# Optimization experiments

Measured on AMD Instinct MI355X. Metric: run time of the kernel, lower is better.

Reference implementation:

```python
import jax, jax.numpy as jnp
import numpy as np

N = 131072      # number of nodes / samples
IN_DIM = 128    # input_dim
H = 128         # hidden_dim
OUT_DIM = 10    # output_dim


def setup_inputs() -> dict:
    key = jax.random.key(0)
    ks = jax.random.split(key, 20)
    s = 0.05
    def rn(k, shape):
        return jax.random.normal(k, shape, jnp.float32) * s
    return {
        "x": jax.random.normal(ks[0], (N, IN_DIM), jnp.float32),
        # GRU layer 1 (seq_len=1, h0=0 => weight_hh contributes nothing; only b_hh matters)
        "w_ih_f1": rn(ks[1], (3 * H, IN_DIM)), "b_ih_f1": rn(ks[2], (3 * H,)), "b_hh_f1": rn(ks[3], (3 * H,)),
        "w_ih_b1": rn(ks[4], (3 * H, IN_DIM)), "b_ih_b1": rn(ks[5], (3 * H,)), "b_hh_b1": rn(ks[6], (3 * H,)),
        # GRU layer 2 (input 2H)
        "w_ih_f2": rn(ks[7], (3 * H, 2 * H)), "b_ih_f2": rn(ks[8], (3 * H,)), "b_hh_f2": rn(ks[9], (3 * H,)),
        "w_ih_b2": rn(ks[10], (3 * H, 2 * H)), "b_ih_b2": rn(ks[11], (3 * H,)), "b_hh_b2": rn(ks[12], (3 * H,)),
        # GCNConv layers
        "w_g1": rn(ks[13], (2 * H, 128)), "b_g1": rn(ks[14], (128,)),
        "w_g2": rn(ks[15], (128, 64)), "b_g2": rn(ks[16], (64,)),
        # final fc
        "w_fc": rn(ks[17], (64, OUT_DIM)), "b_fc": rn(ks[18], (OUT_DIM,)),
    }


def _gru_cell_zero(x, w_ih, b_ih, b_hh):
    # PyTorch GRU cell with h_prev = 0: h' = (1 - z) * n_gate
    gi = x @ w_ih.T + b_ih                    # [n, 3H]
    ir, iz, inn = jnp.split(gi, 3, axis=-1)
    hr, hz, hn = jnp.split(b_hh, 3)
    r = jax.nn.sigmoid(ir + hr)
    z = jax.nn.sigmoid(iz + hz)
    ng = jnp.tanh(inn + r * hn)
    return (1.0 - z) * ng


def _gcn(x, w, b, sources, targets, n):
    # PyG GCNConv: D^{-1/2}(A+I)D^{-1/2} X W + b, self-loops already in edge lists
    xw = x @ w                                 # [n, out]
    deg = jax.ops.segment_sum(jnp.ones(sources.shape[0], x.dtype), targets, num_segments=n)
    dinv = jax.lax.rsqrt(deg)
    norm = dinv[sources] * dinv[targets]       # [E]
    msg = norm[:, None] * xw[sources]          # gather
    return jax.ops.segment_sum(msg, targets, num_segments=n) + b  # scatter-add


def reference(x, w_ih_f1, b_ih_f1, b_hh_f1, w_ih_b1, b_ih_b1, b_hh_b1,
              w_ih_f2, b_ih_f2, b_hh_f2, w_ih_b2, b_ih_b2, b_hh_b2,
              w_g1, b_g1, w_g2, b_g2, w_fc, b_fc):
    n = x.shape[0]
    # seq_len = 1 => bidirectional GRU output is [fwd_cell(x); bwd_cell(x)]
    h1 = jnp.concatenate([_gru_cell_zero(x, w_ih_f1, b_ih_f1, b_hh_f1),
                          _gru_cell_zero(x, w_ih_b1, b_ih_b1, b_hh_b1)], axis=-1)
    h2 = jnp.concatenate([_gru_cell_zero(h1, w_ih_f2, b_ih_f2, b_hh_f2),
                          _gru_cell_zero(h1, w_ih_b2, b_ih_b2, b_hh_b2)], axis=-1)
    # chain graph, both directions, plus self loops (GCNConv adds them)
    src = jnp.arange(n - 1)
    dst = jnp.arange(1, n)
    ar = jnp.arange(n)
    sources = jnp.concatenate([src, dst, ar])
    targets = jnp.concatenate([dst, src, ar])
    g1 = _gcn(h2, w_g1, b_g1, sources, targets, n)   # dropout is identity in eval
    g2 = _gcn(g1, w_g2, b_g2, sources, targets, n)
    return g2 @ w_fc + b_fc
```

## Files before the change

kernel.cpp:

```cpp
#include <hip/hip_runtime.h>
#include <stdint.h>

#define N_NODES 131072
#define HDIM 128

typedef __bf16 bf16x8 __attribute__((ext_vector_type(8)));
typedef float f32x4 __attribute__((ext_vector_type(4)));
typedef unsigned short ushort_t;

__device__ __forceinline__ ushort_t f2bf(float f) {
    union { float f; uint32_t i; } v; v.f = f;
    uint32_t i = v.i;
    return (ushort_t)((i + 0x7FFFu + ((i >> 16) & 1u)) >> 16);
}

__device__ __forceinline__ void gll16(const ushort_t* g, ushort_t* l) {
    __builtin_amdgcn_global_load_lds(
        (const __attribute__((address_space(1))) uint32_t*)g,
        (__attribute__((address_space(3))) uint32_t*)l, 16, 0, 0);
}

__device__ __forceinline__ bf16x8 ldsw(const ushort_t* base, int R, int g) {
    return *(const bf16x8*)&base[R * 64 + (((g - R) & 7) << 3)];
}

__device__ __forceinline__ float fsig(float x) {
    return __builtin_amdgcn_rcpf(1.0f + __expf(-x));
}
__device__ __forceinline__ float ftanh(float y) {
    float yc = fminf(fmaxf(y, -15.0f), 15.0f);
    float e = __expf(2.0f * yc);
    return (e - 1.0f) * __builtin_amdgcn_rcpf(e + 1.0f);
}

template<int NC>
__device__ __forceinline__ void swz(int b, int& m, int& c) {
    int mhi = b / (8 * NC);
    int rem = b - mhi * (8 * NC);
    c = rem >> 3;
    m = mhi * 8 + (rem & 7);
}

__global__ __launch_bounds__(256) void prep_all(
    const float* __restrict__ w_f1, const float* __restrict__ w_b1,
    const float* __restrict__ w_f2, const float* __restrict__ w_b2,
    ushort_t* __restrict__ PWF1, ushort_t* __restrict__ PWB1,
    ushort_t* __restrict__ PWF2, ushort_t* __restrict__ PWB2,
    const float* __restrict__ w_g1, const float* __restrict__ b_g1,
    const float* __restrict__ w_g2, const float* __restrict__ b_g2,
    const float* __restrict__ w_fc, const float* __restrict__ b_fc,
    ushort_t* __restrict__ M16, float* __restrict__ cc)
{
    __shared__ float wfc_s[640];
    __shared__ float T1[128][10];
    const int t = threadIdx.x;

    if (blockIdx.x < 1152) {
        int idx = blockIdx.x * 256 + t;
        if (idx < 49152) {
            PWF1[idx] = f2bf(w_f1[idx]);
        } else if (idx < 98304) {
            int j = idx - 49152;  PWB1[j] = f2bf(w_b1[j]);
        } else if (idx < 196608) {
            int j = idx - 98304;  PWF2[j] = f2bf(w_f2[j]);
        } else if (idx < 294912) {
            int j = idx - 196608; PWB2[j] = f2bf(w_b2[j]);
        }
        return;
    }

    for (int i = t; i < 640; i += 256) wfc_s[i] = w_fc[i];
    __syncthreads();
    if (t < 128) {
        float s[10];
        #pragma unroll
        for (int j = 0; j < 10; ++j) s[j] = 0.0f;
        const float4* row = (const float4*)(w_g2 + t * 64);
        #pragma unroll
        for (int k4 = 0; k4 < 16; ++k4) {
            float4 v = row[k4];
            #pragma unroll
            for (int j = 0; j < 10; ++j)
                s[j] += v.x * wfc_s[(k4 * 4 + 0) * 10 + j] + v.y * wfc_s[(k4 * 4 + 1) * 10 + j]
                      + v.z * wfc_s[(k4 * 4 + 2) * 10 + j] + v.w * wfc_s[(k4 * 4 + 3) * 10 + j];
        }
        #pragma unroll
        for (int j = 0; j < 10; ++j) T1[t][j] = s[j];
    }
    __syncthreads();
    float m[10];
    #pragma unroll
    for (int j = 0; j < 10; ++j) m[j] = 0.0f;
    const float4* row1 = (const float4*)(w_g1 + t * 128);
    #pragma unroll 4
    for (int k4 = 0; k4 < 32; ++k4) {
        float4 v = row1[k4];
        #pragma unroll
        for (int j = 0; j < 10; ++j)
            m[j] += v.x * T1[k4 * 4 + 0][j] + v.y * T1[k4 * 4 + 1][j]
                  + v.z * T1[k4 * 4 + 2][j] + v.w * T1[k4 * 4 + 3][j];
    }
    #pragma unroll
    for (int j = 0; j < 16; ++j)
        M16[j * 256 + t] = (j < 10) ? f2bf(m[j]) : (ushort_t)0;
    if (t < 10) {
        float s1 = 0.0f;
        for (int k2 = 0; k2 < 128; ++k2) s1 += b_g1[k2] * T1[k2][t];
        cc[t] = s1;
        float s2 = 0.0f;
        for (int k3 = 0; k3 < 64; ++k3) s2 += b_g2[k3] * wfc_s[k3 * 10 + t];
        cc[16 + t] = s2 + b_fc[t];
    }
}

__global__ __launch_bounds__(256, 5) void gru_l1(
    const float* __restrict__ X,
    const ushort_t* __restrict__ Wf,
    const ushort_t* __restrict__ Wb,
    const float* __restrict__ bi_f, const float* __restrict__ bh_f,
    const float* __restrict__ bi_b, const float* __restrict__ bh_b,
    ushort_t* __restrict__ Hout)
{
    __shared__ ushort_t As[128 * 64];
    __shared__ ushort_t Bs[96 * 64];
    const int tid = threadIdx.x;
    int mt, comb;
    swz<8>(blockIdx.x, mt, comb);
    const int m0 = mt * 128;
    const int dir = comb >> 2;
    const int j0 = (comb & 3) * 32;
    const ushort_t* W = dir ? Wb : Wf;
    const float* b_ih = dir ? bi_b : bi_f;
    const float* b_hh = dir ? bh_b : bh_f;
    const int coloff = dir << 7;

    const int wv = tid >> 6, lane = tid & 63;
    const int lr = lane & 15, lq = lane >> 4;
    const int tr = tid >> 3, tc = tid & 7;
    const int sc = ((tr + tc) & 7) << 3;

    f32x4 acc[3][2][2];
    #pragma unroll
    for (int g = 0; g < 3; ++g)
        #pragma unroll
        for (int rt = 0; rt < 2; ++rt)
            #pragma unroll
            for (int ct = 0; ct < 2; ++ct)
                #pragma unroll
                for (int e = 0; e < 4; ++e) acc[g][rt][ct][e] = 0.0f;

    for (int t = 0; t < 2; ++t) {
        const int k0 = t * 64;
        const float* ga = X + (size_t)(m0 + tr) * 128 + k0 + sc;
        float4 fa[4][2];
        #pragma unroll
        for (int i = 0; i < 4; ++i) {
            const float4* p = (const float4*)(ga + (size_t)i * 32 * 128);
            fa[i][0] = p[0]; fa[i][1] = p[1];
        }
        #pragma unroll
        for (int i = 0; i < 3; ++i) {
            int wr = (i << 7) + j0 + tr;
            gll16(W + (size_t)wr * 128 + k0 + sc, &Bs[(i * 256 + tid) * 8]);
        }
        #pragma unroll
        for (int i = 0; i < 4; ++i) {
            bf16x8 t8;
            t8[0] = (__bf16)fa[i][0].x; t8[1] = (__bf16)fa[i][0].y;
            t8[2] = (__bf16)fa[i][0].z; t8[3] = (__bf16)fa[i][0].w;
            t8[4] = (__bf16)fa[i][1].x; t8[5] = (__bf16)fa[i][1].y;
            t8[6] = (__bf16)fa[i][1].z; t8[7] = (__bf16)fa[i][1].w;
            *(bf16x8*)&As[(i * 256 + tid) * 8] = t8;
        }
        __syncthreads();
        #pragma unroll
        for (int kk = 0; kk < 64; kk += 32) {
            const int g8 = (kk >> 3) + lq;
            bf16x8 a0 = ldsw(As, wv * 32 + lr, g8);
            bf16x8 a1 = ldsw(As, wv * 32 + 16 + lr, g8);
            #pragma unroll
            for (int g = 0; g < 3; ++g) {
                #pragma unroll
                for (int ct = 0; ct < 2; ++ct) {
                    bf16x8 b = ldsw(Bs, g * 32 + ct * 16 + lr, g8);
                    acc[g][0][ct] = __builtin_amdgcn_mfma_f32_16x16x32_bf16(a0, b, acc[g][0][ct], 0, 0, 0);
                    acc[g][1][ct] = __builtin_amdgcn_mfma_f32_16x16x32_bf16(a1, b, acc[g][1][ct], 0, 0, 0);
                }
            }
        }
        __syncthreads();
    }

    #pragma unroll
    for (int ct = 0; ct < 2; ++ct) {
        const int j = j0 + ct * 16 + lr;
        const float br  = b_ih[j] + b_hh[j];
        const float bz  = b_ih[HDIM + j] + b_hh[HDIM + j];
        const float bn  = b_ih[2 * HDIM + j];
        const float bhn = b_hh[2 * HDIM + j];
        #pragma unroll
        for (int rt = 0; rt < 2; ++rt) {
            #pragma unroll
            for (int r = 0; r < 4; ++r) {
                const int row = m0 + wv * 32 + rt * 16 + lq * 4 + r;
                float rg = fsig(acc[0][rt][ct][r] + br);
                float zg = fsig(acc[1][rt][ct][r] + bz);
                float ng = ftanh(acc[2][rt][ct][r] + bn + rg * bhn);
                ((__bf16*)Hout)[(size_t)row * 256 + coloff + j] = (__bf16)((1.0f - zg) * ng);
            }
        }
    }
}

__global__ __launch_bounds__(256, 5) void gru_l2(
    const ushort_t* __restrict__ A,
    const ushort_t* __restrict__ Wf,
    const ushort_t* __restrict__ Wb,
    const float* __restrict__ bi_f, const float* __restrict__ bh_f,
    const float* __restrict__ bi_b, const float* __restrict__ bh_b,
    const ushort_t* __restrict__ M16,
    float* __restrict__ Zp)
{
    __shared__ ushort_t As[128 * 64];
    __shared__ ushort_t Bs[96 * 64];
    const int tid = threadIdx.x;
    int mt, comb;
    swz<8>(blockIdx.x, mt, comb);
    const int m0 = mt * 128;
    const int dir = comb >> 2;
    const int j0 = (comb & 3) * 32;
    const ushort_t* W = dir ? Wb : Wf;
    const float* b_ih = dir ? bi_b : bi_f;
    const float* b_hh = dir ? bh_b : bh_f;
    const int coloff = dir << 7;

    const int wv = tid >> 6, lane = tid & 63;
    const int lr = lane & 15, lq = lane >> 4;
    const int tr = tid >> 3, tc = tid & 7;
    const int sc = ((tr + tc) & 7) << 3;

    f32x4 acc[3][2][2];
    #pragma unroll
    for (int g = 0; g < 3; ++g)
        #pragma unroll
        for (int rt = 0; rt < 2; ++rt)
            #pragma unroll
            for (int ct = 0; ct < 2; ++ct)
                #pragma unroll
                for (int e = 0; e < 4; ++e) acc[g][rt][ct][e] = 0.0f;

    for (int t = 0; t < 4; ++t) {
        const int k0 = t * 64;
        const ushort_t* ga = A + (size_t)(m0 + tr) * 256 + k0 + sc;
        #pragma unroll
        for (int i = 0; i < 4; ++i)
            gll16(ga + (size_t)i * 32 * 256, &As[(i * 256 + tid) * 8]);
        #pragma unroll
        for (int i = 0; i < 3; ++i) {
            int wr = (i << 7) + j0 + tr;
            gll16(W + (size_t)wr * 256 + k0 + sc, &Bs[(i * 256 + tid) * 8]);
        }
        __syncthreads();
        #pragma unroll
        for (int kk = 0; kk < 64; kk += 32) {
            const int g8 = (kk >> 3) + lq;
            bf16x8 a0 = ldsw(As, wv * 32 + lr, g8);
            bf16x8 a1 = ldsw(As, wv * 32 + 16 + lr, g8);
            #pragma unroll
            for (int g = 0; g < 3; ++g) {
                #pragma unroll
                for (int ct = 0; ct < 2; ++ct) {
                    bf16x8 b = ldsw(Bs, g * 32 + ct * 16 + lr, g8);
                    acc[g][0][ct] = __builtin_amdgcn_mfma_f32_16x16x32_bf16(a0, b, acc[g][0][ct], 0, 0, 0);
                    acc[g][1][ct] = __builtin_amdgcn_mfma_f32_16x16x32_bf16(a1, b, acc[g][1][ct], 0, 0, 0);
                }
            }
        }
        __syncthreads();
    }

    const bf16x8 mb = *(const bf16x8*)&M16[lr * 256 + coloff + j0 + lq * 8];

    ushort_t* hs = &As[wv * 1280];
    #pragma unroll
    for (int ct = 0; ct < 2; ++ct) {
        const int j = j0 + ct * 16 + lr;
        const float br  = b_ih[j] + b_hh[j];
        const float bz  = b_ih[HDIM + j] + b_hh[HDIM + j];
        const float bn  = b_ih[2 * HDIM + j];
        const float bhn = b_hh[2 * HDIM + j];
        #pragma unroll
        for (int rt = 0; rt < 2; ++rt) {
            #pragma unroll
            for (int r = 0; r < 4; ++r) {
                const int lrow = rt * 16 + lq * 4 + r;
                float rg = fsig(acc[0][rt][ct][r] + br);
                float zg = fsig(acc[1][rt][ct][r] + bz);
                float ng = ftanh(acc[2][rt][ct][r] + bn + rg * bhn);
                ((__bf16*)hs)[lrow * 40 + ct * 16 + lr] = (__bf16)((1.0f - zg) * ng);
            }
        }
    }
    __syncthreads();

    bf16x8 ha0 = *(const bf16x8*)&hs[lr * 40 + lq * 8];
    bf16x8 ha1 = *(const bf16x8*)&hs[(16 + lr) * 40 + lq * 8];
    f32x4 z0, z1;
    #pragma unroll
    for (int e = 0; e < 4; ++e) { z0[e] = 0.0f; z1[e] = 0.0f; }
    z0 = __builtin_amdgcn_mfma_f32_16x16x32_bf16(ha0, mb, z0, 0, 0, 0);
    z1 = __builtin_amdgcn_mfma_f32_16x16x32_bf16(ha1, mb, z1, 0, 0, 0);

    if (lr < 10) {
        float* zslice = Zp + (size_t)comb * ((size_t)N_NODES * 10);
        #pragma unroll
        for (int r = 0; r < 4; ++r) {
            zslice[(size_t)(m0 + wv * 32 + lq * 4 + r) * 10 + lr] = z0[r];
            zslice[(size_t)(m0 + wv * 32 + 16 + lq * 4 + r) * 10 + lr] = z1[r];
        }
    }
}

__device__ __forceinline__ float dcoef(int i) {
    return (i == 0 || i == N_NODES - 1) ? 0.70710678118654752f : 0.57735026918962576f;
}
__global__ __launch_bounds__(256) void stz(
    const float* __restrict__ Zp, float* __restrict__ out,
    const float* __restrict__ cc)
{
    __shared__ __align__(16) float zl[2600];
    const int tid = threadIdx.x;
    const int n0 = blockIdx.x * 256;
    const bool edge = (blockIdx.x == 0) || (blockIdx.x == gridDim.x - 1);

    if (!edge) {
        const size_t base4 = ((size_t)n0 * 10 - 20) >> 2;
        const float4* Z4 = (const float4*)Zp;
        for (int i4 = tid; i4 < 650; i4 += 256) {
            float4 a = Z4[base4 + i4];
            #pragma unroll
            for (int s = 1; s < 8; ++s) {
                float4 b = Z4[(size_t)s * ((size_t)N_NODES * 10 / 4) + base4 + i4];
                a.x += b.x; a.y += b.y; a.z += b.z; a.w += b.w;
            }
            ((float4*)zl)[i4] = a;
        }
    } else {
        for (int i = tid; i < 2600; i += 256) {
            int nl = i / 10;
            int c = i - nl * 10;
            int n = n0 - 2 + nl;
            float v = 0.0f;
            if (n >= 0 && n < N_NODES) {
                size_t b = (size_t)n * 10 + c;
                #pragma unroll
                for (int s = 0; s < 8; ++s)
                    v += Zp[(size_t)s * ((size_t)N_NODES * 10) + b];
            }
            zl[i] = v;
        }
    }
    __syncthreads();

    const int i = n0 + tid;
    const float d_i = dcoef(i);
    float dsum = d_i;
    if (i - 1 >= 0) dsum += dcoef(i - 1);
    if (i + 1 < N_NODES) dsum += dcoef(i + 1);

    #pragma unroll
    for (int c = 0; c < 10; ++c) {
        float accv = 0.0f;
        #pragma unroll
        for (int oj = -1; oj <= 1; ++oj) {
            int j = i + oj;
            if (j < 0 || j >= N_NODES) continue;
            float dj = dcoef(j);
            float wj = 0.0f;
            #pragma unroll
            for (int ok = -1; ok <= 1; ++ok) {
                int k = j + ok;
                wj += dcoef(k) * zl[(tid + 2 + oj + ok) * 10 + c];
            }
            accv += dj * dj * wj;
        }
        out[(size_t)i * 10 + c] = d_i * accv + d_i * dsum * cc[c] + cc[16 + c];
    }
}

extern "C" void kernel_launch(void* const* d_in, const int* in_sizes, int n_in,
                              void* d_out, int out_size, void* d_ws, size_t ws_size,
                              hipStream_t stream) {
    const float* x     = (const float*)d_in[0];
    const float* w_f1  = (const float*)d_in[1];
    const float* bi_f1 = (const float*)d_in[2];
    const float* bh_f1 = (const float*)d_in[3];
    const float* w_b1  = (const float*)d_in[4];
    const float* bi_b1 = (const float*)d_in[5];
    const float* bh_b1 = (const float*)d_in[6];
    const float* w_f2  = (const float*)d_in[7];
    const float* bi_f2 = (const float*)d_in[8];
    const float* bh_f2 = (const float*)d_in[9];
    const float* w_b2  = (const float*)d_in[10];
    const float* bi_b2 = (const float*)d_in[11];
    const float* bh_b2 = (const float*)d_in[12];
    const float* w_g1  = (const float*)d_in[13];
    const float* b_g1  = (const float*)d_in[14];
    const float* w_g2  = (const float*)d_in[15];
    const float* b_g2  = (const float*)d_in[16];
    const float* w_fc  = (const float*)d_in[17];
    const float* b_fc  = (const float*)d_in[18];

    char* ws = (char*)d_ws;
    ushort_t* h1   = (ushort_t*)(ws);
    float*    Zp   = (float*)(ws + 67108864);
    ushort_t* PWF1 = (ushort_t*)(ws + 134217728);
    ushort_t* PWB1 = PWF1 + 49152;
    ushort_t* PWF2 = PWB1 + 49152;
    ushort_t* PWB2 = PWF2 + 98304;
    ushort_t* M16  = PWB2 + 98304;
    float*    cc   = (float*)(M16 + 4096);

    prep_all<<<1153, 256, 0, stream>>>(w_f1, w_b1, w_f2, w_b2,
                                       PWF1, PWB1, PWF2, PWB2,
                                       w_g1, b_g1, w_g2, b_g2, w_fc, b_fc,
                                       M16, cc);

    gru_l1<<<N_NODES / 128 * 8, 256, 0, stream>>>(
        x, PWF1, PWB1, bi_f1, bh_f1, bi_b1, bh_b1, h1);
    gru_l2<<<N_NODES / 128 * 8, 256, 0, stream>>>(
        h1, PWF2, PWB2, bi_f2, bh_f2, bi_b2, bh_b2, M16, Zp);

    stz<<<N_NODES / 256, 256, 0, stream>>>(Zp, (float*)d_out, cc);
}
```

Baseline: 280.9 us.

## Double-buffer gru_l2 K-loop with 32-wide stages and manual vmcnt waits

The layer-2 GRU GEMM loop changes from 4 single-buffered 64-wide K stages to 8 double-buffered 32-wide stages. Async global-to-LDS loads for the next stage now overlap the MFMA work on the current one, with explicit s_waitcnt vmcnt counts and raw barriers in place of __syncthreads. It also adds a new LDS swizzle for 32-wide rows and raises wave priority around the MFMAs. The LDS footprint stays about the same, but correctness depends on the hand-tuned vmcnt counts, which differ per wave because of the conditional B load.

```diff
diff --git a/kernel.cpp b/kernel.cpp
--- a/kernel.cpp
+++ b/kernel.cpp
@@ -22,6 +22,10 @@
 
 __device__ __forceinline__ bf16x8 ldsw(const ushort_t* base, int R, int g) {
     return *(const bf16x8*)&base[R * 64 + (((g - R) & 7) << 3)];
+}
+
+__device__ __forceinline__ bf16x8 ldsw32(const ushort_t* base, int R, int g) {
+    return *(const bf16x8*)&base[R * 32 + (((g - (R >> 1)) & 3) << 3)];
 }
 
 __device__ __forceinline__ float fsig(float x) {
@@ -212,6 +216,18 @@
     }
 }
 
+#define L2_STAGE(t_, b_)                                                        \
+    do {                                                                        \
+        const int k0_ = (t_) * 32;                                              \
+        gll16(A + (size_t)(m0 + arow0) * 256 + k0_ + agk0, &As[b_][tid * 8]);   \
+        gll16(A + (size_t)(m0 + arow1) * 256 + k0_ + agk1,                      \
+              &As[b_][(256 + tid) * 8]);                                        \
+        gll16(W + (size_t)bwr0 * 256 + k0_ + bgk0, &Bs[b_][tid * 8]);           \
+        if (tid < 128)                                                          \
+            gll16(W + (size_t)bwr1 * 256 + k0_ + bgk1,                          \
+                  &Bs[b_][(256 + tid) * 8]);                                    \
+    } while (0)
+
 __global__ __launch_bounds__(256, 5) void gru_l2(
     const ushort_t* __restrict__ A,
     const ushort_t* __restrict__ Wf,
@@ -221,8 +237,8 @@
     const ushort_t* __restrict__ M16,
     float* __restrict__ Zp)
 {
-    __shared__ ushort_t As[128 * 64];
-    __shared__ ushort_t Bs[96 * 64];
+    __shared__ ushort_t As[2][128 * 32];
+    __shared__ ushort_t Bs[2][96 * 32];
     const int tid = threadIdx.x;
     int mt, comb;
     swz<8>(blockIdx.x, mt, comb);
@@ -236,8 +252,16 @@
 
     const int wv = tid >> 6, lane = tid & 63;
     const int lr = lane & 15, lq = lane >> 4;
-    const int tr = tid >> 3, tc = tid & 7;
-    const int sc = ((tr + tc) & 7) << 3;
+
+    const int ci0 = tid,        ci1 = 256 + tid;
+    const int arow0 = ci0 >> 2, arow1 = ci1 >> 2;
+    const int agk0 = (((ci0 & 3) + (arow0 >> 1)) & 3) << 3;
+    const int agk1 = (((ci1 & 3) + (arow1 >> 1)) & 3) << 3;
+    const int rb0 = ci0 >> 2,   rb1 = ci1 >> 2;
+    const int bgk0 = (((ci0 & 3) + (rb0 >> 1)) & 3) << 3;
+    const int bgk1 = (((ci1 & 3) + (rb1 >> 1)) & 3) << 3;
+    const int bwr0 = ((rb0 >> 5) << 7) + j0 + (rb0 & 31);
+    const int bwr1 = ((rb1 >> 5) << 7) + j0 + (rb1 & 31);
 
     f32x4 acc[3][2][2];
     #pragma unroll
@@ -249,39 +273,45 @@
                 #pragma unroll
                 for (int e = 0; e < 4; ++e) acc[g][rt][ct][e] = 0.0f;
 
-    for (int t = 0; t < 4; ++t) {
-        const int k0 = t * 64;
-        const ushort_t* ga = A + (size_t)(m0 + tr) * 256 + k0 + sc;
-        #pragma unroll
-        for (int i = 0; i < 4; ++i)
-            gll16(ga + (size_t)i * 32 * 256, &As[(i * 256 + tid) * 8]);
-        #pragma unroll
-        for (int i = 0; i < 3; ++i) {
-            int wr = (i << 7) + j0 + tr;
-            gll16(W + (size_t)wr * 256 + k0 + sc, &Bs[(i * 256 + tid) * 8]);
-        }
-        __syncthreads();
-        #pragma unroll
-        for (int kk = 0; kk < 64; kk += 32) {
-            const int g8 = (kk >> 3) + lq;
-            bf16x8 a0 = ldsw(As, wv * 32 + lr, g8);
-            bf16x8 a1 = ldsw(As, wv * 32 + 16 + lr, g8);
+    L2_STAGE(0, 0);
+    L2_STAGE(1, 1);
+
+    #pragma unroll
+    for (int t = 0; t < 8; ++t) {
+        const int b = t & 1;
+        if (t < 7) {
+            if (wv < 2) asm volatile("s_waitcnt vmcnt(4)" ::: "memory");
+            else        asm volatile("s_waitcnt vmcnt(3)" ::: "memory");
+        } else {
+            asm volatile("s_waitcnt vmcnt(0)" ::: "memory");
+        }
+        __builtin_amdgcn_s_barrier();
+        __builtin_amdgcn_sched_barrier(0);
+        {
+            const ushort_t* Ac = &As[b][0];
+            const ushort_t* Bc = &Bs[b][0];
+            bf16x8 a0 = ldsw32(Ac, wv * 32 + lr, lq);
+            bf16x8 a1 = ldsw32(Ac, wv * 32 + 16 + lr, lq);
+            __builtin_amdgcn_s_setprio(1);
             #pragma unroll
             for (int g = 0; g < 3; ++g) {
                 #pragma unroll
                 for (int ct = 0; ct < 2; ++ct) {
-                    bf16x8 b = ldsw(Bs, g * 32 + ct * 16 + lr, g8);
-                    acc[g][0][ct] = __builtin_amdgcn_mfma_f32_16x16x32_bf16(a0, b, acc[g][0][ct], 0, 0, 0);
-                    acc[g][1][ct] = __builtin_amdgcn_mfma_f32_16x16x32_bf16(a1, b, acc[g][1][ct], 0, 0, 0);
+                    bf16x8 bb = ldsw32(Bc, g * 32 + ct * 16 + lr, lq);
+                    acc[g][0][ct] = __builtin_amdgcn_mfma_f32_16x16x32_bf16(a0, bb, acc[g][0][ct], 0, 0, 0);
+                    acc[g][1][ct] = __builtin_amdgcn_mfma_f32_16x16x32_bf16(a1, bb, acc[g][1][ct], 0, 0, 0);
                 }
             }
-        }
-        __syncthreads();
+            __builtin_amdgcn_s_setprio(0);
+        }
+        __builtin_amdgcn_sched_barrier(0);
+        __builtin_amdgcn_s_barrier();
+        if (t + 2 < 8) L2_STAGE(t + 2, b);
     }
 
     const bf16x8 mb = *(const bf16x8*)&M16[lr * 256 + coloff + j0 + lq * 8];
 
-    ushort_t* hs = &As[wv * 1280];
+    ushort_t* hs = &As[0][0] + wv * 1280;
     #pragma unroll
     for (int ct = 0; ct < 2; ++ct) {
         const int j = j0 + ct * 16 + lr;
```

Result: no change. 281.0 us (+0.0%).

## Stage X tile once per block in gru_l1 and loop over all output column chunks

Applied to the files above, without the earlier changes.

gru_l1 now launches one 512-thread block per 128-row tile. Each block converts the full 128x128 fp32 X tile to bf16 in LDS once, then loops over all 8 direction/column chunks, streaming the weight slices through LDS. Previously 8 separate blocks each re-read and re-converted the same X rows. The trade is fewer, larger blocks with a serial inner loop over chunks, more LDS per block (32KB for A), and an extra sync per chunk.

```diff
diff --git a/kernel.cpp b/kernel.cpp
--- a/kernel.cpp
+++ b/kernel.cpp
@@ -113,7 +113,7 @@
     }
 }
 
-__global__ __launch_bounds__(256, 5) void gru_l1(
+__global__ __launch_bounds__(512, 4) void gru_l1(
     const float* __restrict__ X,
     const ushort_t* __restrict__ Wf,
     const ushort_t* __restrict__ Wb,
@@ -121,91 +121,87 @@
     const float* __restrict__ bi_b, const float* __restrict__ bh_b,
     ushort_t* __restrict__ Hout)
 {
-    __shared__ ushort_t As[128 * 64];
+    __shared__ ushort_t As[2 * 8192];
     __shared__ ushort_t Bs[96 * 64];
     const int tid = threadIdx.x;
-    int mt, comb;
-    swz<8>(blockIdx.x, mt, comb);
-    const int m0 = mt * 128;
-    const int dir = comb >> 2;
-    const int j0 = (comb & 3) * 32;
-    const ushort_t* W = dir ? Wb : Wf;
-    const float* b_ih = dir ? bi_b : bi_f;
-    const float* b_hh = dir ? bh_b : bh_f;
-    const int coloff = dir << 7;
-
+    const int m0 = blockIdx.x * 128;
     const int wv = tid >> 6, lane = tid & 63;
     const int lr = lane & 15, lq = lane >> 4;
-    const int tr = tid >> 3, tc = tid & 7;
-    const int sc = ((tr + tc) & 7) << 3;
-
-    f32x4 acc[3][2][2];
-    #pragma unroll
-    for (int g = 0; g < 3; ++g)
-        #pragma unroll
-        for (int rt = 0; rt < 2; ++rt)
+
+    #pragma unroll
+    for (int p = 0; p < 4; ++p) {
+        int ci = p * 512 + tid;
+        int reg = ci >> 10, w = ci & 1023, row = w >> 3, slot = w & 7;
+        int g = (slot + row) & 7;
+        const float* src = X + (size_t)(m0 + row) * 128 + reg * 64 + g * 8;
+        float4 f0 = ((const float4*)src)[0];
+        float4 f1 = ((const float4*)src)[1];
+        bf16x8 t8;
+        t8[0] = (__bf16)f0.x; t8[1] = (__bf16)f0.y; t8[2] = (__bf16)f0.z; t8[3] = (__bf16)f0.w;
+        t8[4] = (__bf16)f1.x; t8[5] = (__bf16)f1.y; t8[6] = (__bf16)f1.z; t8[7] = (__bf16)f1.w;
+        *(bf16x8*)&As[ci * 8] = t8;
+    }
+    __syncthreads();
+
+    for (int jc = 0; jc < 8; ++jc) {
+        const int dir = jc >> 2;
+        const int j0 = (jc & 3) * 32;
+        const ushort_t* W = dir ? Wb : Wf;
+        const float* b_ih = dir ? bi_b : bi_f;
+        const float* b_hh = dir ? bh_b : bh_f;
+        const int coloff = dir << 7;
+
+        f32x4 acc[3][2];
+        #pragma unroll
+        for (int g = 0; g < 3; ++g)
             #pragma unroll
             for (int ct = 0; ct < 2; ++ct)
                 #pragma unroll
-                for (int e = 0; e < 4; ++e) acc[g][rt][ct][e] = 0.0f;
-
-    for (int t = 0; t < 2; ++t) {
-        const int k0 = t * 64;
-        const float* ga = X + (size_t)(m0 + tr) * 128 + k0 + sc;
-        float4 fa[4][2];
-        #pragma unroll
-        for (int i = 0; i < 4; ++i) {
-            const float4* p = (const float4*)(ga + (size_t)i * 32 * 128);
-            fa[i][0] = p[0]; fa[i][1] = p[1];
-        }
-        #pragma unroll
-        for (int i = 0; i < 3; ++i) {
-            int wr = (i << 7) + j0 + tr;
-            gll16(W + (size_t)wr * 128 + k0 + sc, &Bs[(i * 256 + tid) * 8]);
-        }
-        #pragma unroll
-        for (int i = 0; i < 4; ++i) {
-            bf16x8 t8;
-            t8[0] = (__bf16)fa[i][0].x; t8[1] = (__bf16)fa[i][0].y;
-            t8[2] = (__bf16)fa[i][0].z; t8[3] = (__bf16)fa[i][0].w;
-            t8[4] = (__bf16)fa[i][1].x; t8[5] = (__bf16)fa[i][1].y;
-            t8[6] = (__bf16)fa[i][1].z; t8[7] = (__bf16)fa[i][1].w;
-            *(bf16x8*)&As[(i * 256 + tid) * 8] = t8;
-        }
-        __syncthreads();
-        #pragma unroll
-        for (int kk = 0; kk < 64; kk += 32) {
-            const int g8 = (kk >> 3) + lq;
-            bf16x8 a0 = ldsw(As, wv * 32 + lr, g8);
-            bf16x8 a1 = ldsw(As, wv * 32 + 16 + lr, g8);
-            #pragma unroll
-            for (int g = 0; g < 3; ++g) {
+                for (int e = 0; e < 4; ++e) acc[g][ct][e] = 0.0f;
+
+        for (int t = 0; t < 2; ++t) {
+            {
+                int ci = tid;
+                int r96 = ci >> 3, slot = ci & 7, g = (slot + r96) & 7;
+                int wr = ((r96 >> 5) << 7) + j0 + (r96 & 31);
+                gll16(W + (size_t)wr * 128 + t * 64 + g * 8, &Bs[ci * 8]);
+                if (tid < 256) {
+                    int ci2 = 512 + tid;
+                    int r2 = ci2 >> 3, s2 = ci2 & 7, g2 = (s2 + r2) & 7;
+                    int wr2 = ((r2 >> 5) << 7) + j0 + (r2 & 31);
+                    gll16(W + (size_t)wr2 * 128 + t * 64 + g2 * 8, &Bs[ci2 * 8]);
+                }
+            }
+            __syncthreads();
+            #pragma unroll
+            for (int kk = 0; kk < 64; kk += 32) {
+                const int g8 = (kk >> 3) + lq;
+                bf16x8 a0 = ldsw(&As[t * 8192], wv * 16 + lr, g8);
                 #pragma unroll
-                for (int ct = 0; ct < 2; ++ct) {
-                    bf16x8 b = ldsw(Bs, g * 32 + ct * 16 + lr, g8);
-                    acc[g][0][ct] = __builtin_amdgcn_mfma_f32_16x16x32_bf16(a0, b, acc[g][0][ct], 0, 0, 0);
-                    acc[g][1][ct] = __builtin_amdgcn_mfma_f32_16x16x32_bf16(a1, b, acc[g][1][ct], 0, 0, 0);
+                for (int g = 0; g < 3; ++g) {
+                    #pragma unroll
+                    for (int ct = 0; ct < 2; ++ct) {
+                        bf16x8 b = ldsw(Bs, g * 32 + ct * 16 + lr, g8);
+                        acc[g][ct] = __builtin_amdgcn_mfma_f32_16x16x32_bf16(a0, b, acc[g][ct], 0, 0, 0);
+                    }
                 }
             }
-        }
-        __syncthreads();
-    }
-
-    #pragma unroll
-    for (int ct = 0; ct < 2; ++ct) {
-        const int j = j0 + ct * 16 + lr;
-        const float br  = b_ih[j] + b_hh[j];
-        const float bz  = b_ih[HDIM + j] + b_hh[HDIM + j];
-        const float bn  = b_ih[2 * HDIM + j];
-        const float bhn = b_hh[2 * HDIM + j];
-        #pragma unroll
-        for (int rt = 0; rt < 2; ++rt) {
+            __syncthreads();
+        }
+
+        #pragma unroll
+        for (int ct = 0; ct < 2; ++ct) {
+            const int j = j0 + ct * 16 + lr;
+            const float br  = b_ih[j] + b_hh[j];
+            const float bz  = b_ih[HDIM + j] + b_hh[HDIM + j];
+            const float bn  = b_ih[2 * HDIM + j];
+            const float bhn = b_hh[2 * HDIM + j];
             #pragma unroll
             for (int r = 0; r < 4; ++r) {
-                const int row = m0 + wv * 32 + rt * 16 + lq * 4 + r;
-                float rg = fsig(acc[0][rt][ct][r] + br);
-                float zg = fsig(acc[1][rt][ct][r] + bz);
-                float ng = ftanh(acc[2][rt][ct][r] + bn + rg * bhn);
+                const int row = m0 + wv * 16 + lq * 4 + r;
+                float rg = fsig(acc[0][ct][r] + br);
+                float zg = fsig(acc[1][ct][r] + bz);
+                float ng = ftanh(acc[2][ct][r] + bn + rg * bhn);
                 ((__bf16*)Hout)[(size_t)row * 256 + coloff + j] = (__bf16)((1.0f - zg) * ng);
             }
         }
@@ -426,7 +422,7 @@
                                        w_g1, b_g1, w_g2, b_g2, w_fc, b_fc,
                                        M16, cc);
 
-    gru_l1<<<N_NODES / 128 * 8, 256, 0, stream>>>(
+    gru_l1<<<N_NODES / 128, 512, 0, stream>>>(
         x, PWF1, PWB1, bi_f1, bh_f1, bi_b1, bh_b1, h1);
     gru_l2<<<N_NODES / 128 * 8, 256, 0, stream>>>(
         h1, PWF2, PWB2, bi_f2, bh_f2, bi_b2, bh_b2, M16, Zp);
```

Measured after the change: 277.0 us. About the same (-1.4%).
